# Optimization experiments

Measured on AMD Instinct MI355X. Metric: run time of the kernel, lower is better.

The kernel has to match this reference:

```python
import jax, jax.numpy as jnp
import numpy as np

HEADS = 8
DIM_HEAD = 64
DIM = 512
EPS = 1e-5


def setup_inputs() -> dict:
    key = jax.random.key(0)
    ks = jax.random.split(key, 4)
    b, n = 4, 2048
    inner = HEADS * DIM_HEAD
    x = jax.random.normal(ks[0], (b, n, DIM), dtype=jnp.float32)
    pose_bias = jax.random.normal(ks[1], (b, n), dtype=jnp.float32)
    ln_gamma = jnp.ones((DIM,), dtype=jnp.float32)
    ln_beta = jnp.zeros((DIM,), dtype=jnp.float32)
    w_qkv = jax.random.normal(ks[2], (DIM, 3 * inner), dtype=jnp.float32) * (DIM ** -0.5)
    w_out = jax.random.normal(ks[3], (inner, DIM), dtype=jnp.float32) * (inner ** -0.5)
    beta = jnp.float32(0.5)
    return {"x": x, "pose_bias": pose_bias, "ln_gamma": ln_gamma,
            "ln_beta": ln_beta, "w_qkv": w_qkv, "w_out": w_out, "beta": beta}


def reference(x, pose_bias, ln_gamma, ln_beta, w_qkv, w_out, beta):
    b, n, d = x.shape
    h, dh = HEADS, DIM_HEAD
    scale = dh ** -0.5
    # LayerNorm (biased variance, eps=1e-5, affine)
    mu = jnp.mean(x, axis=-1, keepdims=True)
    var = jnp.mean(jnp.square(x - mu), axis=-1, keepdims=True)
    xn = (x - mu) * jax.lax.rsqrt(var + EPS) * ln_gamma + ln_beta
    # fused QKV projection (no bias)
    qkv = xn @ w_qkv                                  # [b, n, 3*h*dh]
    q, k, v = jnp.split(qkv, 3, axis=-1)
    def to_heads(t):
        return t.reshape(b, n, h, dh).transpose(0, 2, 1, 3)  # [b, h, n, dh]
    q, k, v = to_heads(q), to_heads(k), to_heads(v)
    dots = jnp.einsum('bhnd,bhmd->bhnm', q, k) * scale  # [b, h, n, n]
    # additive pose bias: beta * (bias_i + bias_j), broadcast over heads
    pose_attn = beta * (pose_bias[:, None, :, None] + pose_bias[:, None, None, :])
    dots = dots + pose_attn
    attn = jax.nn.softmax(dots, axis=-1)
    out = jnp.einsum('bhnm,bhmd->bhnd', attn, v)       # [b, h, n, dh]
    out = out.transpose(0, 2, 1, 3).reshape(b, n, h * dh)
    return out @ w_out
```

## Files before the change

### kernel.cpp

```cpp
#include <hip/hip_runtime.h>

#define NH    8
#define DH    64
#define DIMD  512
#define NCTX  2048
#define NB    4
#define NROWS (NB * NCTX)
#define QKVN  (3 * DIMD)

typedef __attribute__((ext_vector_type(8))) short bf16x8;
typedef __attribute__((ext_vector_type(4))) float f32x4;

#define INV_LN2 1.44269504f
#define SCLOG   (0.125f * INV_LN2)

__device__ __forceinline__ unsigned short f2bits(float f) {
  unsigned u = __float_as_uint(f);
  u += 0x7fffu + ((u >> 16) & 1u);
  return (unsigned short)(u >> 16);
}
__device__ __forceinline__ float bits2f(unsigned short u) {
  return __uint_as_float(((unsigned)u) << 16);
}

__device__ __forceinline__ void gll16(const void* g, void* l) {
  __builtin_amdgcn_global_load_lds(
      (const __attribute__((address_space(1))) unsigned int*)g,
      (__attribute__((address_space(3))) unsigned int*)l, 16, 0, 0);
}
__device__ __forceinline__ void gll4(const void* g, void* l) {
  __builtin_amdgcn_global_load_lds(
      (const __attribute__((address_space(1))) unsigned int*)g,
      (__attribute__((address_space(3))) unsigned int*)l, 4, 0, 0);
}

__global__ __launch_bounds__(256) void lntc_kernel(
    const float* __restrict__ x,
    const float* __restrict__ gamma,
    const float* __restrict__ beta,
    unsigned short* __restrict__ xn,
    const float* __restrict__ in0, unsigned short* __restrict__ out0,
    const float* __restrict__ in1, unsigned short* __restrict__ out1,
    const float* __restrict__ pb, const float* __restrict__ betap,
    float* __restrict__ pbl) {
  __shared__ float T[64][65];
  if (blockIdx.x < 2048) {
    const int wid  = threadIdx.x >> 6;
    const int lane = threadIdx.x & 63;
    const int row  = blockIdx.x * 4 + wid;
    const float* xr = x + (size_t)row * DIMD + lane * 8;
    float v[8];
    const float4 a = *reinterpret_cast<const float4*>(xr);
    const float4 b = *reinterpret_cast<const float4*>(xr + 4);
    v[0] = a.x; v[1] = a.y; v[2] = a.z; v[3] = a.w;
    v[4] = b.x; v[5] = b.y; v[6] = b.z; v[7] = b.w;
    float s = 0.f;
#pragma unroll
    for (int i = 0; i < 8; ++i) s += v[i];
#pragma unroll
    for (int off = 32; off; off >>= 1) s += __shfl_down(s, off);
    s = __shfl(s, 0);
    const float mu = s * (1.f / DIMD);
    float ss = 0.f;
#pragma unroll
    for (int i = 0; i < 8; ++i) { float d = v[i] - mu; ss += d * d; }
#pragma unroll
    for (int off = 32; off; off >>= 1) ss += __shfl_down(ss, off);
    ss = __shfl(ss, 0);
    const float inv = rsqrtf(ss * (1.f / DIMD) + 1e-5f);
    const float4 g0 = *reinterpret_cast<const float4*>(gamma + lane * 8);
    const float4 g1 = *reinterpret_cast<const float4*>(gamma + lane * 8 + 4);
    const float4 b0 = *reinterpret_cast<const float4*>(beta + lane * 8);
    const float4 b1 = *reinterpret_cast<const float4*>(beta + lane * 8 + 4);
    float g[8] = {g0.x, g0.y, g0.z, g0.w, g1.x, g1.y, g1.z, g1.w};
    float be[8] = {b0.x, b0.y, b0.z, b0.w, b1.x, b1.y, b1.z, b1.w};
    bf16x8 o;
#pragma unroll
    for (int i = 0; i < 8; ++i)
      o[i] = (short)f2bits((v[i] - mu) * inv * g[i] + be[i]);
    *reinterpret_cast<bf16x8*>(xn + (size_t)row * DIMD + lane * 8) = o;
  } else if (blockIdx.x < 2432) {
    const int t = blockIdx.x - 2048;
    const int bx = t % 24, rest = t / 24;
    const int by = rest % 8, z = rest / 8;
    const int C = z ? DIMD : QKVN;
    if (z && bx >= DIMD / 64) return;
    const float* in = z ? in1 : in0;
    unsigned short* out = z ? out1 : out0;
    const int r0 = by * 64, c0 = bx * 64;
    const int ty = threadIdx.x >> 4, tx = threadIdx.x & 15;
#pragma unroll
    for (int i = 0; i < 4; ++i) {
      const int r = ty + i * 16;
      const float4 v = *reinterpret_cast<const float4*>(
          in + (size_t)(r0 + r) * C + c0 + tx * 4);
      T[r][tx * 4 + 0] = v.x; T[r][tx * 4 + 1] = v.y;
      T[r][tx * 4 + 2] = v.z; T[r][tx * 4 + 3] = v.w;
    }
    __syncthreads();
#pragma unroll
    for (int i = 0; i < 4; ++i) {
      const int c = ty + i * 16;
      ushort4 o;
      o.x = f2bits(T[tx * 4 + 0][c]); o.y = f2bits(T[tx * 4 + 1][c]);
      o.z = f2bits(T[tx * 4 + 2][c]); o.w = f2bits(T[tx * 4 + 3][c]);
      *reinterpret_cast<ushort4*>(out + (size_t)(c0 + c) * DIMD + r0 + tx * 4) = o;
    }
  } else {
    const int t2 = blockIdx.x - 2432;
    const float bl2 = betap[0] * INV_LN2;
    const int idx = t2 * 2048 + threadIdx.x * 8;
    const float4 a = *reinterpret_cast<const float4*>(pb + idx);
    const float4 b = *reinterpret_cast<const float4*>(pb + idx + 4);
    float4 oa = {bl2 * a.x, bl2 * a.y, bl2 * a.z, bl2 * a.w};
    float4 ob = {bl2 * b.x, bl2 * b.y, bl2 * b.z, bl2 * b.w};
    *reinterpret_cast<float4*>(pbl + idx) = oa;
    *reinterpret_cast<float4*>(pbl + idx + 4) = ob;
  }
}

__device__ __forceinline__ void storeC(float* C, size_t idx, float v) { C[idx] = v; }
__device__ __forceinline__ void storeC(unsigned short* C, size_t idx, float v) { C[idx] = f2bits(v); }

template <typename CT, bool QS>
__global__ __launch_bounds__(256) void ggemm_kernel(
    const unsigned short* __restrict__ A, const unsigned short* __restrict__ Bt,
    CT* __restrict__ C, unsigned short* __restrict__ vtg, int M, int N, int K) {
  __shared__ __align__(16) unsigned short As[128 * 64];
  __shared__ __align__(16) unsigned short Bs[128 * 64];
  const int tid  = threadIdx.x;
  const int wave = tid >> 6, lane = tid & 63;
  const int quad = lane >> 4, l16 = lane & 15;
  const int wr = wave >> 1, wc = wave & 1;
  const int tm0 = blockIdx.y * 128, tn0 = blockIdx.x * 128;
  const bool vswap = QS && (tn0 >= 2 * DIMD);
  const int srow = wave * 8 + (lane >> 3);
  const int ssh  = (((lane & 7) * 16) ^ ((lane >> 3) << 4)) >> 1;
  const unsigned short* ap = A + (size_t)(tm0 + srow) * K + ssh;
  const unsigned short* bp = Bt + (size_t)(tn0 + srow) * K + ssh;
  const int xs = (l16 & 7) << 3;
  f32x4 acc[4][4];
#pragma unroll
  for (int i = 0; i < 4; ++i)
#pragma unroll
    for (int j = 0; j < 4; ++j) acc[i][j] = (f32x4){0.f, 0.f, 0.f, 0.f};

  for (int k0 = 0; k0 < K; k0 += 64) {
#pragma unroll
    for (int i = 0; i < 4; ++i) {
      gll16(ap + (size_t)(i * 32) * K + k0, &As[i * 2048 + wave * 512]);
      gll16(bp + (size_t)(i * 32) * K + k0, &Bs[i * 2048 + wave * 512]);
    }
    __syncthreads();
#pragma unroll
    for (int kc = 0; kc < 2; ++kc) {
      const int kk = ((kc * 32 + quad * 8) ^ xs);
      bf16x8 af[4], bfr[4];
#pragma unroll
      for (int i = 0; i < 4; ++i)
        af[i] = *reinterpret_cast<const bf16x8*>(&As[(wr * 64 + i * 16 + l16) * 64 + kk]);
#pragma unroll
      for (int j = 0; j < 4; ++j)
        bfr[j] = *reinterpret_cast<const bf16x8*>(&Bs[(wc * 64 + j * 16 + l16) * 64 + kk]);
      if (vswap) {
#pragma unroll
        for (int i = 0; i < 4; ++i)
#pragma unroll
          for (int j = 0; j < 4; ++j)
            acc[i][j] = __builtin_amdgcn_mfma_f32_16x16x32_bf16(bfr[j], af[i], acc[i][j], 0, 0, 0);
      } else {
#pragma unroll
        for (int i = 0; i < 4; ++i)
#pragma unroll
          for (int j = 0; j < 4; ++j)
            acc[i][j] = __builtin_amdgcn_mfma_f32_16x16x32_bf16(af[i], bfr[j], acc[i][j], 0, 0, 0);
      }
    }
    __syncthreads();
  }
  if (vswap) {
#pragma unroll
    for (int j = 0; j < 4; ++j)
#pragma unroll
      for (int i = 0; i < 4; ++i)
#pragma unroll
        for (int r = 0; r < 4; ++r) {
          const int vcol = tn0 - 2 * DIMD + wc * 64 + j * 16 + quad * 4 + r;
          const int hi = vcol >> 6, d = vcol & 63;
          const int rowc = tm0 + wr * 64 + i * 16 + l16;
          const int bi = rowc >> 11, jc = rowc & (NCTX - 1);
          vtg[((size_t)(bi * NH + hi) * DH + d) * NCTX + jc] = f2bits(acc[i][j][r]);
        }
  } else {
#pragma unroll
    for (int j = 0; j < 4; ++j) {
      const int col = tn0 + wc * 64 + j * 16 + l16;
      const float scl = (QS && col < DIMD) ? SCLOG : 1.0f;
#pragma unroll
      for (int i = 0; i < 4; ++i)
#pragma unroll
        for (int r = 0; r < 4; ++r)
          storeC(C, (size_t)(tm0 + wr * 64 + i * 16 + quad * 4 + r) * N + col,
                 acc[i][j][r] * scl);
    }
  }
}

template <typename CT, bool QS>
__global__ __launch_bounds__(256) void mgemm_kernel(
    const unsigned short* __restrict__ A, const unsigned short* __restrict__ Bt,
    CT* __restrict__ C, int M, int N, int K) {
  __shared__ __align__(16) unsigned short As[128][72];
  __shared__ __align__(16) unsigned short Bs[128][72];
  const int tid  = threadIdx.x;
  const int wave = tid >> 6, lane = tid & 63;
  const int quad = lane >> 4, l16 = lane & 15;
  const int wr = wave >> 1, wc = wave & 1;
  const int tm0 = blockIdx.y * 128, tn0 = blockIdx.x * 128;
  const int srow = tid >> 3;
  const int schunk = (tid & 7) * 8;
  f32x4 acc[4][4];
#pragma unroll
  for (int i = 0; i < 4; ++i)
#pragma unroll
    for (int j = 0; j < 4; ++j) acc[i][j] = (f32x4){0.f, 0.f, 0.f, 0.f};

  bf16x8 ra[4], rb[4];
#pragma unroll
  for (int p = 0; p < 4; ++p) {
    const int r = srow + p * 32;
    ra[p] = *reinterpret_cast<const bf16x8*>(A + (size_t)(tm0 + r) * K + schunk);
    rb[p] = *reinterpret_cast<const bf16x8*>(Bt + (size_t)(tn0 + r) * K + schunk);
  }
  for (int k0 = 0; k0 < K; k0 += 64) {
#pragma unroll
    for (int p = 0; p < 4; ++p) {
      const int r = srow + p * 32;
      *reinterpret_cast<bf16x8*>(&As[r][schunk]) = ra[p];
      *reinterpret_cast<bf16x8*>(&Bs[r][schunk]) = rb[p];
    }
    __syncthreads();
    if (k0 + 64 < K) {
#pragma unroll
      for (int p = 0; p < 4; ++p) {
        const int r = srow + p * 32;
        ra[p] = *reinterpret_cast<const bf16x8*>(A + (size_t)(tm0 + r) * K + k0 + 64 + schunk);
        rb[p] = *reinterpret_cast<const bf16x8*>(Bt + (size_t)(tn0 + r) * K + k0 + 64 + schunk);
      }
    }
#pragma unroll
    for (int kc = 0; kc < 2; ++kc) {
      const int kk = kc * 32 + quad * 8;
      bf16x8 af[4], bfr[4];
#pragma unroll
      for (int i = 0; i < 4; ++i)
        af[i] = *reinterpret_cast<const bf16x8*>(&As[wr * 64 + i * 16 + l16][kk]);
#pragma unroll
      for (int j = 0; j < 4; ++j)
        bfr[j] = *reinterpret_cast<const bf16x8*>(&Bs[wc * 64 + j * 16 + l16][kk]);
#pragma unroll
      for (int i = 0; i < 4; ++i)
#pragma unroll
        for (int j = 0; j < 4; ++j)
          acc[i][j] = __builtin_amdgcn_mfma_f32_16x16x32_bf16(af[i], bfr[j], acc[i][j], 0, 0, 0);
    }
    __syncthreads();
  }
#pragma unroll
  for (int j = 0; j < 4; ++j) {
    const int col = tn0 + wc * 64 + j * 16 + l16;
    const float scl = (QS && col < DIMD) ? SCLOG : 1.0f;
#pragma unroll
    for (int i = 0; i < 4; ++i)
#pragma unroll
      for (int r = 0; r < 4; ++r)
        storeC(C, (size_t)(tm0 + wr * 64 + i * 16 + quad * 4 + r) * N + col,
               acc[i][j][r] * scl);
  }
}

__global__ __launch_bounds__(256, 4) void fattn_kernel(
    const unsigned short* __restrict__ qkv,
    const unsigned short* __restrict__ vtg,
    const float* __restrict__ pbl,
    unsigned short* __restrict__ out) {
  __shared__ __align__(16) unsigned short lds[2][8320];

  const int qt = blockIdx.x, hi = blockIdx.y, bi = blockIdx.z;
  const int tid  = threadIdx.x;
  const int wave = tid >> 6, lane = tid & 63;
  const int quad = lane >> 4, l16 = lane & 15;
  const int wq = wave & 1, wk = wave >> 1;
  const int qrow0 = qt * 64;
  const unsigned short* base  = qkv + (size_t)bi * NCTX * QKVN + hi * DH;
  const unsigned short* vbase = vtg + (size_t)(bi * NH + hi) * DH * NCTX;
  const float* pbase = pbl + (size_t)bi * NCTX;

  const int sr8 = lane >> 3;
  const int ssh = ((((lane & 7) * 16) ^ (sr8 << 4)) >> 1);
  const unsigned short* kp0 = base + (size_t)(wave * 8 + sr8) * QKVN + DIMD + ssh;
  const unsigned short* kp1 = kp0 + (size_t)32 * QKVN;
  const unsigned short* vp0 = vbase + (size_t)(wave * 8 + sr8) * NCTX + ssh;
  const unsigned short* vp1 = vp0 + (size_t)32 * NCTX;
  const float* pp = pbase + lane;

#define STAGE(buf)                                    \
  gll16(kp0, &(buf)[wave * 512]);                     \
  gll16(kp1, &(buf)[2048 + wave * 512]);              \
  gll16(vp0, &(buf)[4096 + wave * 512]);              \
  gll16(vp1, &(buf)[6144 + wave * 512]);              \
  if (tid < 64) gll4(pp, &(buf)[8192]);               \
  kp0 += (size_t)64 * QKVN; kp1 += (size_t)64 * QKVN; \
  vp0 += 64; vp1 += 64; pp += 64;

  bf16x8 qf[2][2];
#pragma unroll
  for (int u = 0; u < 2; ++u)
#pragma unroll
    for (int h = 0; h < 2; ++h)
      qf[u][h] = *reinterpret_cast<const bf16x8*>(
          base + (size_t)(qrow0 + wq * 32 + u * 16 + l16) * QKVN + h * 32 + quad * 8);

  const int xs = (l16 & 7) << 3;
  const int kofs0 = (wk * 32 + l16) * 64 + ((quad * 8) ^ xs);
  const int kofs1 = (wk * 32 + l16) * 64 + ((32 + quad * 8) ^ xs);
  const int vofs  = 4096 + l16 * 64 + ((wk * 32 + quad * 8) ^ xs);
  const int pofs  = wk * 32 + quad * 4;

  const bf16x8 ones = {16256, 16256, 16256, 16256, 16256, 16256, 16256, 16256};

  STAGE(lds[0]);
  __syncthreads();

  f32x4 O[2][4], accl[2];
#pragma unroll
  for (int u = 0; u < 2; ++u) {
    accl[u] = (f32x4){0.f, 0.f, 0.f, 0.f};
#pragma unroll
    for (int s = 0; s < 4; ++s) O[u][s] = (f32x4){0.f, 0.f, 0.f, 0.f};
  }

  for (int kt = 0; kt < 32; ++kt) {
    const unsigned short* bc = lds[kt & 1];
    if (kt < 31) { STAGE(lds[(kt & 1) ^ 1]); }
    const float* pblf = (const float*)(bc + 8192);
    f32x4 sfr[2][2];
#pragma unroll
    for (int t = 0; t < 2; ++t) {
      const bf16x8 kf0 = *reinterpret_cast<const bf16x8*>(&bc[kofs0 + t * 1024]);
      const bf16x8 kf1 = *reinterpret_cast<const bf16x8*>(&bc[kofs1 + t * 1024]);
      const f32x4 bias = *reinterpret_cast<const f32x4*>(&pblf[pofs + t * 16]);
#pragma unroll
      for (int u = 0; u < 2; ++u) {
        f32x4 acc = bias;
        acc = __builtin_amdgcn_mfma_f32_16x16x32_bf16(kf0, qf[u][0], acc, 0, 0, 0);
        acc = __builtin_amdgcn_mfma_f32_16x16x32_bf16(kf1, qf[u][1], acc, 0, 0, 0);
        sfr[t][u] = acc;
      }
    }
    bf16x8 pf[2];
#pragma unroll
    for (int u = 0; u < 2; ++u) {
      const unsigned a0 = __float_as_uint(__builtin_amdgcn_exp2f(sfr[0][u][0])) + 0x8000u;
      const unsigned a1 = __float_as_uint(__builtin_amdgcn_exp2f(sfr[0][u][1])) + 0x8000u;
      const unsigned a2 = __float_as_uint(__builtin_amdgcn_exp2f(sfr[0][u][2])) + 0x8000u;
      const unsigned a3 = __float_as_uint(__builtin_amdgcn_exp2f(sfr[0][u][3])) + 0x8000u;
      const unsigned b0 = __float_as_uint(__builtin_amdgcn_exp2f(sfr[1][u][0])) + 0x8000u;
      const unsigned b1 = __float_as_uint(__builtin_amdgcn_exp2f(sfr[1][u][1])) + 0x8000u;
      const unsigned b2 = __float_as_uint(__builtin_amdgcn_exp2f(sfr[1][u][2])) + 0x8000u;
      const unsigned b3 = __float_as_uint(__builtin_amdgcn_exp2f(sfr[1][u][3])) + 0x8000u;
      unsigned x0 = __builtin_amdgcn_perm(a1, a0, 0x07060302u);
      unsigned x1 = __builtin_amdgcn_perm(a3, a2, 0x07060302u);
      unsigned y0 = __builtin_amdgcn_perm(b1, b0, 0x07060302u);
      unsigned y1 = __builtin_amdgcn_perm(b3, b2, 0x07060302u);
      asm("v_permlane32_swap_b32 %0, %1" : "+v"(x0), "+v"(y0));
      asm("v_permlane32_swap_b32 %0, %1" : "+v"(x1), "+v"(y1));
      asm("v_permlane16_swap_b32 %0, %1" : "+v"(x0), "+v"(y0));
      asm("v_permlane16_swap_b32 %0, %1" : "+v"(x1), "+v"(y1));
      union { unsigned q[4]; bf16x8 v; } pu;
      pu.q[0] = x0; pu.q[1] = x1; pu.q[2] = y0; pu.q[3] = y1;
      pf[u] = pu.v;
    }
    {
      accl[0] = __builtin_amdgcn_mfma_f32_16x16x32_bf16(pf[0], ones, accl[0], 0, 0, 0);
      accl[1] = __builtin_amdgcn_mfma_f32_16x16x32_bf16(pf[1], ones, accl[1], 0, 0, 0);
#pragma unroll
      for (int s = 0; s < 4; ++s) {
        const bf16x8 bv = *reinterpret_cast<const bf16x8*>(&bc[vofs + s * 1024]);
        O[0][s] = __builtin_amdgcn_mfma_f32_16x16x32_bf16(pf[0], bv, O[0][s], 0, 0, 0);
        O[1][s] = __builtin_amdgcn_mfma_f32_16x16x32_bf16(pf[1], bv, O[1][s], 0, 0, 0);
      }
    }
    __syncthreads();
  }
#undef STAGE
  unsigned short* Ob = (unsigned short*)lds;
  float* lb = (float*)((unsigned short*)lds + 4352);
  if (wk == 1) {
#pragma unroll
    for (int u = 0; u < 2; ++u) {
#pragma unroll
      for (int s = 0; s < 4; ++s)
#pragma unroll
        for (int r = 0; r < 4; ++r)
          Ob[(wq * 32 + u * 16 + quad * 4 + r) * 68 + s * 16 + l16] = f2bits(O[u][s][r]);
      if (l16 == 0)
#pragma unroll
        for (int r = 0; r < 4; ++r)
          lb[64 + wq * 32 + u * 16 + quad * 4 + r] = accl[u][r];
    }
  } else {
#pragma unroll
    for (int u = 0; u < 2; ++u)
      if (l16 == 0)
#pragma unroll
        for (int r = 0; r < 4; ++r)
          lb[wq * 32 + u * 16 + quad * 4 + r] = accl[u][r];
  }
  __syncthreads();
  if (wk == 0) {
#pragma unroll
    for (int u = 0; u < 2; ++u)
#pragma unroll
      for (int r = 0; r < 4; ++r) {
        const int ql = wq * 32 + u * 16 + quad * 4 + r;
        const float linv = 1.f / (lb[ql] + lb[64 + ql]);
        const size_t orow = ((size_t)bi * NCTX + qrow0 + ql) * DIMD + hi * DH;
#pragma unroll
        for (int s = 0; s < 4; ++s)
          out[orow + s * 16 + l16] =
              f2bits((O[u][s][r] + bits2f(Ob[ql * 68 + s * 16 + l16])) * linv);
      }
  }
}

extern "C" void kernel_launch(void* const* d_in, const int* in_sizes, int n_in,
                              void* d_out, int out_size, void* d_ws, size_t ws_size,
                              hipStream_t stream) {
  const float* x     = (const float*)d_in[0];
  const float* pose  = (const float*)d_in[1];
  const float* gam   = (const float*)d_in[2];
  const float* bet   = (const float*)d_in[3];
  const float* wqkv  = (const float*)d_in[4];
  const float* wout  = (const float*)d_in[5];
  const float* betap = (const float*)d_in[6];
  float* out = (float*)d_out;

  unsigned short* xn    = (unsigned short*)d_ws;
  unsigned short* qkvb  = xn + (size_t)NROWS * DIMD;
  unsigned short* wqkvT = qkvb + (size_t)NROWS * QKVN;
  unsigned short* woutT = wqkvT + (size_t)QKVN * DIMD;
  unsigned short* vtg   = woutT + (size_t)DIMD * DIMD;
  float*          pbl   = (float*)(vtg + (size_t)NB * NH * DH * NCTX);
  unsigned short* aout  = xn;

  lntc_kernel<<<2048 + 384 + 4, 256, 0, stream>>>(
      x, gam, bet, xn, wqkv, wqkvT, wout, woutT, pose, betap, pbl);
  ggemm_kernel<unsigned short, true><<<dim3(QKVN / 128, NROWS / 128), 256, 0, stream>>>(
      xn, wqkvT, qkvb, vtg, NROWS, QKVN, DIMD);
  fattn_kernel<<<dim3(NCTX / 64, NH, NB), 256, 0, stream>>>(qkvb, vtg, pbl, aout);
  mgemm_kernel<float, false><<<dim3(DIMD / 128, NROWS / 128), 256, 0, stream>>>(
      aout, woutT, out, NROWS, DIMD, DIMD);
}
```

Measured before the change: 166.3 us.

## Load V and pose bias directly from global memory instead of staging through LDS

The attention kernel stops staging V tiles and the pose bias vector into shared memory. Each lane now reads its V fragments and bias values straight from global memory, and LDS holds only K. This halves LDS use per block, which can raise occupancy and removes LDS traffic for V. The cost is uncoalesced 16-byte global loads on the critical path with no prefetch. Separately, the manual bf16 pack via add-and-perm is replaced by the HIP float2-to-bfloat162 conversion intrinsic.

Measured after the change: 191.5 us. +15.2%, slower.

```diff
diff --git a/kernel.cpp b/kernel.cpp
--- a/kernel.cpp
+++ b/kernel.cpp
@@ -1,4 +1,5 @@
 #include <hip/hip_runtime.h>
+#include <hip/hip_bf16.h>
 
 #define NH    8
 #define DH    64
@@ -22,16 +23,15 @@
 __device__ __forceinline__ float bits2f(unsigned short u) {
   return __uint_as_float(((unsigned)u) << 16);
 }
+__device__ __forceinline__ unsigned pk2(float lo, float hi) {
+  __hip_bfloat162 h = __float22bfloat162_rn(float2{lo, hi});
+  union { __hip_bfloat162 h; unsigned u; } c; c.h = h; return c.u;
+}
 
 __device__ __forceinline__ void gll16(const void* g, void* l) {
   __builtin_amdgcn_global_load_lds(
       (const __attribute__((address_space(1))) unsigned int*)g,
       (__attribute__((address_space(3))) unsigned int*)l, 16, 0, 0);
-}
-__device__ __forceinline__ void gll4(const void* g, void* l) {
-  __builtin_amdgcn_global_load_lds(
-      (const __attribute__((address_space(1))) unsigned int*)g,
-      (__attribute__((address_space(3))) unsigned int*)l, 4, 0, 0);
 }
 
 __global__ __launch_bounds__(256) void lntc_kernel(
@@ -284,7 +284,7 @@
     const unsigned short* __restrict__ vtg,
     const float* __restrict__ pbl,
     unsigned short* __restrict__ out) {
-  __shared__ __align__(16) unsigned short lds[2][8320];
+  __shared__ __align__(16) unsigned short lds[2][4096];
 
   const int qt = blockIdx.x, hi = blockIdx.y, bi = blockIdx.z;
   const int tid  = threadIdx.x;
@@ -294,24 +294,16 @@
   const int qrow0 = qt * 64;
   const unsigned short* base  = qkv + (size_t)bi * NCTX * QKVN + hi * DH;
   const unsigned short* vbase = vtg + (size_t)(bi * NH + hi) * DH * NCTX;
-  const float* pbase = pbl + (size_t)bi * NCTX;
 
   const int sr8 = lane >> 3;
   const int ssh = ((((lane & 7) * 16) ^ (sr8 << 4)) >> 1);
   const unsigned short* kp0 = base + (size_t)(wave * 8 + sr8) * QKVN + DIMD + ssh;
   const unsigned short* kp1 = kp0 + (size_t)32 * QKVN;
-  const unsigned short* vp0 = vbase + (size_t)(wave * 8 + sr8) * NCTX + ssh;
-  const unsigned short* vp1 = vp0 + (size_t)32 * NCTX;
-  const float* pp = pbase + lane;
 
 #define STAGE(buf)                                    \
   gll16(kp0, &(buf)[wave * 512]);                     \
   gll16(kp1, &(buf)[2048 + wave * 512]);              \
-  gll16(vp0, &(buf)[4096 + wave * 512]);              \
-  gll16(vp1, &(buf)[6144 + wave * 512]);              \
-  if (tid < 64) gll4(pp, &(buf)[8192]);               \
-  kp0 += (size_t)64 * QKVN; kp1 += (size_t)64 * QKVN; \
-  vp0 += 64; vp1 += 64; pp += 64;
+  kp0 += (size_t)64 * QKVN; kp1 += (size_t)64 * QKVN;
 
   bf16x8 qf[2][2];
 #pragma unroll
@@ -324,8 +316,8 @@
   const int xs = (l16 & 7) << 3;
   const int kofs0 = (wk * 32 + l16) * 64 + ((quad * 8) ^ xs);
   const int kofs1 = (wk * 32 + l16) * 64 + ((32 + quad * 8) ^ xs);
-  const int vofs  = 4096 + l16 * 64 + ((wk * 32 + quad * 8) ^ xs);
-  const int pofs  = wk * 32 + quad * 4;
+  const unsigned short* vg = vbase + (size_t)l16 * NCTX + wk * 32 + quad * 8;
+  const float* pg = pbl + (size_t)bi * NCTX + wk * 32 + quad * 4;
 
   const bf16x8 ones = {16256, 16256, 16256, 16256, 16256, 16256, 16256, 16256};
 
@@ -343,13 +335,14 @@
   for (int kt = 0; kt < 32; ++kt) {
     const unsigned short* bc = lds[kt & 1];
     if (kt < 31) { STAGE(lds[(kt & 1) ^ 1]); }
-    const float* pblf = (const float*)(bc + 8192);
+    const unsigned short* vgk = vg + kt * 64;
+    const float* pgk = pg + kt * 64;
     f32x4 sfr[2][2];
 #pragma unroll
     for (int t = 0; t < 2; ++t) {
       const bf16x8 kf0 = *reinterpret_cast<const bf16x8*>(&bc[kofs0 + t * 1024]);
       const bf16x8 kf1 = *reinterpret_cast<const bf16x8*>(&bc[kofs1 + t * 1024]);
-      const f32x4 bias = *reinterpret_cast<const f32x4*>(&pblf[pofs + t * 16]);
+      const f32x4 bias = *reinterpret_cast<const f32x4*>(pgk + t * 16);
 #pragma unroll
       for (int u = 0; u < 2; ++u) {
         f32x4 acc = bias;
@@ -361,18 +354,14 @@
     bf16x8 pf[2];
 #pragma unroll
     for (int u = 0; u < 2; ++u) {
-      const unsigned a0 = __float_as_uint(__builtin_amdgcn_exp2f(sfr[0][u][0])) + 0x8000u;
-      const unsigned a1 = __float_as_uint(__builtin_amdgcn_exp2f(sfr[0][u][1])) + 0x8000u;
-      const unsigned a2 = __float_as_uint(__builtin_amdgcn_exp2f(sfr[0][u][2])) + 0x8000u;
-      const unsigned a3 = __float_as_uint(__builtin_amdgcn_exp2f(sfr[0][u][3])) + 0x8000u;
-      const unsigned b0 = __float_as_uint(__builtin_amdgcn_exp2f(sfr[1][u][0])) + 0x8000u;
-      const unsigned b1 = __float_as_uint(__builtin_amdgcn_exp2f(sfr[1][u][1])) + 0x8000u;
-      const unsigned b2 = __float_as_uint(__builtin_amdgcn_exp2f(sfr[1][u][2])) + 0x8000u;
-      const unsigned b3 = __float_as_uint(__builtin_amdgcn_exp2f(sfr[1][u][3])) + 0x8000u;
-      unsigned x0 = __builtin_amdgcn_perm(a1, a0, 0x07060302u);
-      unsigned x1 = __builtin_amdgcn_perm(a3, a2, 0x07060302u);
-      unsigned y0 = __builtin_amdgcn_perm(b1, b0, 0x07060302u);
-      unsigned y1 = __builtin_amdgcn_perm(b3, b2, 0x07060302u);
+      unsigned x0 = pk2(__builtin_amdgcn_exp2f(sfr[0][u][0]),
+                        __builtin_amdgcn_exp2f(sfr[0][u][1]));
+      unsigned x1 = pk2(__builtin_amdgcn_exp2f(sfr[0][u][2]),
+                        __builtin_amdgcn_exp2f(sfr[0][u][3]));
+      unsigned y0 = pk2(__builtin_amdgcn_exp2f(sfr[1][u][0]),
+                        __builtin_amdgcn_exp2f(sfr[1][u][1]));
+      unsigned y1 = pk2(__builtin_amdgcn_exp2f(sfr[1][u][2]),
+                        __builtin_amdgcn_exp2f(sfr[1][u][3]));
       asm("v_permlane32_swap_b32 %0, %1" : "+v"(x0), "+v"(y0));
       asm("v_permlane32_swap_b32 %0, %1" : "+v"(x1), "+v"(y1));
       asm("v_permlane16_swap_b32 %0, %1" : "+v"(x0), "+v"(y0));
@@ -386,7 +375,8 @@
       accl[1] = __builtin_amdgcn_mfma_f32_16x16x32_bf16(pf[1], ones, accl[1], 0, 0, 0);
 #pragma unroll
       for (int s = 0; s < 4; ++s) {
-        const bf16x8 bv = *reinterpret_cast<const bf16x8*>(&bc[vofs + s * 1024]);
+        const bf16x8 bv = *reinterpret_cast<const bf16x8*>(
+            vgk + (size_t)s * 16 * NCTX);
         O[0][s] = __builtin_amdgcn_mfma_f32_16x16x32_bf16(pf[0], bv, O[0][s], 0, 0, 0);
         O[1][s] = __builtin_amdgcn_mfma_f32_16x16x32_bf16(pf[1], bv, O[1][s], 0, 0, 0);
       }
```
